# Optimization experiments

Hardware: AMD Instinct MI355X
Metric: run time of the kernel (lower is better)

Reference implementation:

```python
import jax, jax.numpy as jnp
import numpy as np

# Hardcoded capability requirements per task (3 capabilities x 13 tasks), as in the source.
CAP_MATRIX = 0.01 * np.array([
    [0.0, 33.0, 50.0, 43.0, 56.0, 67.0, 62.0, 47.0, 50.0, 51.0, 64.0, 64.0, 68.0],
    [0.0, 33.0, 49.0, 39.0, 58.0, 67.0, 60.0, 54.0, 52.0, 52.0, 67.0, 69.0, 71.0],
    [0.0, 33.0, 42.0, 39.0, 44.0, 52.0, 49.0, 42.0, 45.0, 46.0, 52.0, 53.0, 56.0],
], dtype=np.float32)  # [3, 13]

T_TASKS = 64      # tasks per observation sequence
B_SEQS = 262144   # number of observation sequences
N_TASK_IDS = 13
CAP_DIM = 3


def setup_inputs() -> dict:
    key = jax.random.key(0)
    k1, k2, k3, k4, k5 = jax.random.split(key, 5)
    # Performance encoding must avoid the invalid (1,1) combo:
    # state 0 -> (0,0) no info; state 1 -> (0,1) success; state 2 -> (1,0) failure.
    state = jax.random.randint(k1, (T_TASKS, B_SEQS), 0, 3)
    inptasksperf = jnp.stack(
        [(state == 2).astype(jnp.int32), (state == 1).astype(jnp.int32)], axis=-1
    )  # [T, B, 2]
    tasksobsids = jax.random.randint(k2, (T_TASKS, B_SEQS, 1), 0, N_TASK_IDS).astype(jnp.int32)
    taskspredids = jax.random.randint(k3, (B_SEQS, 1), 0, N_TASK_IDS).astype(jnp.int32)
    inptasksobs = jnp.zeros((T_TASKS, B_SEQS, 1), jnp.float32)  # only shapes are used
    betas = 20.0 * jax.random.uniform(k4, (CAP_DIM,), jnp.float32)
    zetas = jax.random.uniform(k5, (CAP_DIM,), jnp.float32)
    return {
        "inptasksobs": inptasksobs,
        "inptasksperf": inptasksperf,
        "tasksobsids": tasksobsids,
        "taskspredids": taskspredids,
        "num_obs_tasks": T_TASKS,
        "betas": betas,
        "zetas": zetas,
    }


def reference(inptasksobs, inptasksperf, tasksobsids, taskspredids, num_obs_tasks, betas, zetas):
    cap_table = jnp.asarray(CAP_MATRIX.T)                # [13, 3] per-task capability rows
    obs_cap = cap_table[tasksobsids[..., 0]]             # [T, B, 3]
    p0 = inptasksperf[..., 0] != 0                       # [T, B]
    p1 = inptasksperf[..., 1] != 0
    success = jnp.logical_and(~p0, p1)                   # (0,1) -> success
    failure = jnp.logical_and(p0, ~p1)                   # (1,0) -> failure; (0,0) -> skip

    def step(cap, x):
        oc, s, f = x                                     # oc [B,3], s/f [B]
        cap = jnp.where(s[:, None], jnp.maximum(cap, oc), cap)
        cap = jnp.where(f[:, None], jnp.minimum(cap, oc), cap)
        return cap, None

    cap0 = jnp.zeros((obs_cap.shape[1], CAP_DIM), jnp.float32)
    cap, _ = jax.lax.scan(step, cap0, (obs_cap, success, failure))  # [B, 3]

    req = cap_table[taskspredids[:, 0]]                  # [B, 3]
    p = betas * (req - cap)                              # [B, 3]
    trust = jnp.prod((1.0 + jnp.exp(p)) ** (-zetas), axis=-1, keepdims=True)  # [B, 1]
    return trust
```

## Files before the change

### kernel.cpp

```cpp
#include <hip/hip_runtime.h>

#define T_TASKS 64
#define B_SEQS 262144
#define BLOCK 256
#define CHUNKS 4
#define TPC 16
#define PAIRS 64

#define POS_BIG  3.402823466e+38f
#define NEG_BIG -3.402823466e+38f

typedef int v4i __attribute__((ext_vector_type(4)));
typedef int v2i __attribute__((ext_vector_type(2)));

__constant__ float c_capT[13][4] = {
    {0.00f, 0.00f, 0.00f, 0.f}, {0.33f, 0.33f, 0.33f, 0.f},
    {0.50f, 0.49f, 0.42f, 0.f}, {0.43f, 0.39f, 0.39f, 0.f},
    {0.56f, 0.58f, 0.44f, 0.f}, {0.67f, 0.67f, 0.52f, 0.f},
    {0.62f, 0.60f, 0.49f, 0.f}, {0.47f, 0.54f, 0.42f, 0.f},
    {0.50f, 0.52f, 0.45f, 0.f}, {0.51f, 0.52f, 0.46f, 0.f},
    {0.64f, 0.67f, 0.52f, 0.f}, {0.64f, 0.69f, 0.53f, 0.f},
    {0.68f, 0.71f, 0.56f, 0.f},
};

#define STEP(l, h, A, B)                          \
    l = __builtin_amdgcn_fmed3f(l, A, B);         \
    h = __builtin_amdgcn_fmed3f(h, A, B);

#define GLOAD4(dst, ptr) \
    asm volatile("global_load_dwordx4 %0, %1, off" : "=v"(dst) : "v"(ptr))
#define GLOAD2(dst, ptr) \
    asm volatile("global_load_dwordx2 %0, %1, off" : "=v"(dst) : "v"(ptr))
#define WAITC(N)                                                  \
    asm volatile("s_waitcnt vmcnt(" #N ")" ::: "memory");         \
    __builtin_amdgcn_sched_barrier(0);

__global__ __launch_bounds__(BLOCK, 4) void trust_kernel(
    const v4i* __restrict__ perf2,
    const v2i* __restrict__ obs2,
    const int* __restrict__ predids,
    const float* __restrict__ betas,
    const float* __restrict__ zetas,
    float* __restrict__ out)
{
    __shared__ float4 s_cap[13];
    __shared__ float  s_lh[CHUNKS][2 * PAIRS][7];

    if (threadIdx.x < 13)
        s_cap[threadIdx.x] = *(const float4*)&c_capT[threadIdx.x][0];
    __syncthreads();

    const int tid = threadIdx.x;
    const int wv  = tid >> 6;
    const int ln  = tid & 63;
    const size_t RS = B_SEQS / 2;
    const size_t pairBase = (size_t)blockIdx.x * PAIRS;

    const v4i* ap = perf2 + (size_t)(wv * TPC) * RS + pairBase + ln;
    const v2i* bp = obs2  + (size_t)(wv * TPC) * RS + pairBase + ln;

    v4i pfs0, pfs1, pfs2, pfs3;
    v2i ids0, ids1, ids2, ids3;

#define ISSUE(S)                                   \
    GLOAD4(pfs##S, ap);  ap += RS;                 \
    GLOAD2(ids##S, bp);  bp += RS;

    float la0=NEG_BIG, la1=NEG_BIG, la2=NEG_BIG;
    float ha0=POS_BIG, ha1=POS_BIG, ha2=POS_BIG;
    float lb0=NEG_BIG, lb1=NEG_BIG, lb2=NEG_BIG;
    float hb0=POS_BIG, hb1=POS_BIG, hb2=POS_BIG;

#define CONSUME(pf, idv)                                                     \
    {                                                                        \
        const float4 oa = s_cap[(idv).x];                                    \
        const float4 ob = s_cap[(idv).y];                                    \
        const bool sa = ((pf).x == 0) && ((pf).y != 0);                      \
        const bool fa = ((pf).x != 0) && ((pf).y == 0);                      \
        const bool sb = ((pf).z == 0) && ((pf).w != 0);                      \
        const bool fb = ((pf).z != 0) && ((pf).w == 0);                      \
        const float Aa0 = sa ? oa.x : NEG_BIG, Ba0 = fa ? oa.x : POS_BIG;    \
        const float Aa1 = sa ? oa.y : NEG_BIG, Ba1 = fa ? oa.y : POS_BIG;    \
        const float Aa2 = sa ? oa.z : NEG_BIG, Ba2 = fa ? oa.z : POS_BIG;    \
        const float Ab0 = sb ? ob.x : NEG_BIG, Bb0 = fb ? ob.x : POS_BIG;    \
        const float Ab1 = sb ? ob.y : NEG_BIG, Bb1 = fb ? ob.y : POS_BIG;    \
        const float Ab2 = sb ? ob.z : NEG_BIG, Bb2 = fb ? ob.z : POS_BIG;    \
        STEP(la0, ha0, Aa0, Ba0)                                             \
        STEP(la1, ha1, Aa1, Ba1)                                             \
        STEP(la2, ha2, Aa2, Ba2)                                             \
        STEP(lb0, hb0, Ab0, Bb0)                                             \
        STEP(lb1, hb1, Ab1, Bb1)                                             \
        STEP(lb2, hb2, Ab2, Bb2)                                             \
    }

    ISSUE(0) ISSUE(1) ISSUE(2) ISSUE(3)
    WAITC(6) CONSUME(pfs0, ids0) ISSUE(0)
    WAITC(6) CONSUME(pfs1, ids1) ISSUE(1)
    WAITC(6) CONSUME(pfs2, ids2) ISSUE(2)
    WAITC(6) CONSUME(pfs3, ids3) ISSUE(3)
    WAITC(6) CONSUME(pfs0, ids0) ISSUE(0)
    WAITC(6) CONSUME(pfs1, ids1) ISSUE(1)
    WAITC(6) CONSUME(pfs2, ids2) ISSUE(2)
    WAITC(6) CONSUME(pfs3, ids3) ISSUE(3)
    WAITC(6) CONSUME(pfs0, ids0) ISSUE(0)
    WAITC(6) CONSUME(pfs1, ids1) ISSUE(1)
    WAITC(6) CONSUME(pfs2, ids2) ISSUE(2)
    WAITC(6) CONSUME(pfs3, ids3) ISSUE(3)
    WAITC(6) CONSUME(pfs0, ids0)
    WAITC(4) CONSUME(pfs1, ids1)
    WAITC(2) CONSUME(pfs2, ids2)
    WAITC(0) CONSUME(pfs3, ids3)
#undef CONSUME
#undef ISSUE

    float* da = &s_lh[wv][2 * ln][0];
    da[0]=la0; da[1]=la1; da[2]=la2; da[3]=ha0; da[4]=ha1; da[5]=ha2;
    float* db = &s_lh[wv][2 * ln + 1][0];
    db[0]=lb0; db[1]=lb1; db[2]=lb2; db[3]=hb0; db[4]=hb1; db[5]=hb2;
    __syncthreads();

    if (tid < 2 * PAIRS) {
        float x0 = 0.0f, x1 = 0.0f, x2 = 0.0f;
        #pragma unroll
        for (int cc = 0; cc < CHUNKS; ++cc) {
            const float* q = &s_lh[cc][tid][0];
            x0 = fminf(fmaxf(x0, q[0]), q[3]);
            x1 = fminf(fmaxf(x1, q[1]), q[4]);
            x2 = fminf(fmaxf(x2, q[2]), q[5]);
        }
        const size_t seq = (size_t)blockIdx.x * (2 * PAIRS) + tid;
        const int pid = predids[seq];
        const float4 r = s_cap[pid];

        const float q0 = betas[0] * (r.x - x0);
        const float q1 = betas[1] * (r.y - x1);
        const float q2 = betas[2] * (r.z - x2);

        const float t0 = powf(1.0f + expf(q0), -zetas[0]);
        const float t1 = powf(1.0f + expf(q1), -zetas[1]);
        const float t2 = powf(1.0f + expf(q2), -zetas[2]);

        out[seq] = t0 * t1 * t2;
    }
}

extern "C" void kernel_launch(void* const* d_in, const int* in_sizes, int n_in,
                              void* d_out, int out_size, void* d_ws, size_t ws_size,
                              hipStream_t stream) {
    const v4i*   perf2   = (const v4i*)d_in[1];
    const v2i*   obs2    = (const v2i*)d_in[2];
    const int*   predids = (const int*)d_in[3];
    const float* betas   = (const float*)d_in[5];
    const float* zetas   = (const float*)d_in[6];
    float* out = (float*)d_out;

    const int blocks = B_SEQS / (2 * PAIRS);
    trust_kernel<<<blocks, BLOCK, 0, stream>>>(perf2, obs2, predids, betas, zetas, out);
}
```

Baseline: 267.5 us.

## Process two pair-columns per thread to double work per block and halve grid

Doubles PAIRS so each thread handles two adjacent 64-pair column groups, issuing two loads per slot and keeping four sets of min/max accumulators, with pipeline depth reduced from four slots to two. The final reduction now uses all 256 threads instead of half. This aims to raise memory-level parallelism per wave and reduce block count and idle threads in the epilogue, at the cost of more registers and shared memory per block (occupancy risk at launch bounds 4).

```diff
diff --git a/kernel.cpp b/kernel.cpp
--- a/kernel.cpp
+++ b/kernel.cpp
@@ -5,7 +5,7 @@
 #define BLOCK 256
 #define CHUNKS 4
 #define TPC 16
-#define PAIRS 64
+#define PAIRS 128
 
 #define POS_BIG  3.402823466e+38f
 #define NEG_BIG -3.402823466e+38f
@@ -56,70 +56,86 @@
     const size_t RS = B_SEQS / 2;
     const size_t pairBase = (size_t)blockIdx.x * PAIRS;
 
-    const v4i* ap = perf2 + (size_t)(wv * TPC) * RS + pairBase + ln;
-    const v2i* bp = obs2  + (size_t)(wv * TPC) * RS + pairBase + ln;
+    const v4i* ap0 = perf2 + (size_t)(wv * TPC) * RS + pairBase + ln;
+    const v4i* ap1 = ap0 + 64;
+    const v2i* bp0 = obs2  + (size_t)(wv * TPC) * RS + pairBase + ln;
+    const v2i* bp1 = bp0 + 64;
 
-    v4i pfs0, pfs1, pfs2, pfs3;
-    v2i ids0, ids1, ids2, ids3;
+    v4i pfA0, pfB0, pfA1, pfB1;
+    v2i idA0, idB0, idA1, idB1;
 
-#define ISSUE(S)                                   \
-    GLOAD4(pfs##S, ap);  ap += RS;                 \
-    GLOAD2(ids##S, bp);  bp += RS;
+#define ISSUE(S)                                        \
+    GLOAD4(pfA##S, ap0);  GLOAD4(pfB##S, ap1);          \
+    ap0 += RS;  ap1 += RS;                              \
+    GLOAD2(idA##S, bp0);  GLOAD2(idB##S, bp1);          \
+    bp0 += RS;  bp1 += RS;
 
-    float la0=NEG_BIG, la1=NEG_BIG, la2=NEG_BIG;
-    float ha0=POS_BIG, ha1=POS_BIG, ha2=POS_BIG;
-    float lb0=NEG_BIG, lb1=NEG_BIG, lb2=NEG_BIG;
-    float hb0=POS_BIG, hb1=POS_BIG, hb2=POS_BIG;
+    float la0=NEG_BIG, la1=NEG_BIG, la2=NEG_BIG, ha0=POS_BIG, ha1=POS_BIG, ha2=POS_BIG;
+    float lb0=NEG_BIG, lb1=NEG_BIG, lb2=NEG_BIG, hb0=POS_BIG, hb1=POS_BIG, hb2=POS_BIG;
+    float lc0=NEG_BIG, lc1=NEG_BIG, lc2=NEG_BIG, hc0=POS_BIG, hc1=POS_BIG, hc2=POS_BIG;
+    float ld0=NEG_BIG, ld1=NEG_BIG, ld2=NEG_BIG, hd0=POS_BIG, hd1=POS_BIG, hd2=POS_BIG;
 
-#define CONSUME(pf, idv)                                                     \
+#define CONSUME12(pf, idv, l0,l1,l2,h0,h1,h2, m0,m1,m2,g0,g1,g2)             \
     {                                                                        \
         const float4 oa = s_cap[(idv).x];                                    \
         const float4 ob = s_cap[(idv).y];                                    \
-        const bool sa = ((pf).x == 0) && ((pf).y != 0);                      \
-        const bool fa = ((pf).x != 0) && ((pf).y == 0);                      \
-        const bool sb = ((pf).z == 0) && ((pf).w != 0);                      \
-        const bool fb = ((pf).z != 0) && ((pf).w == 0);                      \
-        const float Aa0 = sa ? oa.x : NEG_BIG, Ba0 = fa ? oa.x : POS_BIG;    \
-        const float Aa1 = sa ? oa.y : NEG_BIG, Ba1 = fa ? oa.y : POS_BIG;    \
-        const float Aa2 = sa ? oa.z : NEG_BIG, Ba2 = fa ? oa.z : POS_BIG;    \
-        const float Ab0 = sb ? ob.x : NEG_BIG, Bb0 = fb ? ob.x : POS_BIG;    \
-        const float Ab1 = sb ? ob.y : NEG_BIG, Bb1 = fb ? ob.y : POS_BIG;    \
-        const float Ab2 = sb ? ob.z : NEG_BIG, Bb2 = fb ? ob.z : POS_BIG;    \
-        STEP(la0, ha0, Aa0, Ba0)                                             \
-        STEP(la1, ha1, Aa1, Ba1)                                             \
-        STEP(la2, ha2, Aa2, Ba2)                                             \
-        STEP(lb0, hb0, Ab0, Bb0)                                             \
-        STEP(lb1, hb1, Ab1, Bb1)                                             \
-        STEP(lb2, hb2, Ab2, Bb2)                                             \
+        const bool sx = ((pf).x == 0) && ((pf).y != 0);                      \
+        const bool fx = ((pf).x != 0) && ((pf).y == 0);                      \
+        const bool sy = ((pf).z == 0) && ((pf).w != 0);                      \
+        const bool fy = ((pf).z != 0) && ((pf).w == 0);                      \
+        const float Ax0 = sx ? oa.x : NEG_BIG, Bx0 = fx ? oa.x : POS_BIG;    \
+        const float Ax1 = sx ? oa.y : NEG_BIG, Bx1 = fx ? oa.y : POS_BIG;    \
+        const float Ax2 = sx ? oa.z : NEG_BIG, Bx2 = fx ? oa.z : POS_BIG;    \
+        const float Ay0 = sy ? ob.x : NEG_BIG, By0 = fy ? ob.x : POS_BIG;    \
+        const float Ay1 = sy ? ob.y : NEG_BIG, By1 = fy ? ob.y : POS_BIG;    \
+        const float Ay2 = sy ? ob.z : NEG_BIG, By2 = fy ? ob.z : POS_BIG;    \
+        STEP(l0, h0, Ax0, Bx0)                                               \
+        STEP(l1, h1, Ax1, Bx1)                                               \
+        STEP(l2, h2, Ax2, Bx2)                                               \
+        STEP(m0, g0, Ay0, By0)                                               \
+        STEP(m1, g1, Ay1, By1)                                               \
+        STEP(m2, g2, Ay2, By2)                                               \
     }
 
-    ISSUE(0) ISSUE(1) ISSUE(2) ISSUE(3)
-    WAITC(6) CONSUME(pfs0, ids0) ISSUE(0)
-    WAITC(6) CONSUME(pfs1, ids1) ISSUE(1)
-    WAITC(6) CONSUME(pfs2, ids2) ISSUE(2)
-    WAITC(6) CONSUME(pfs3, ids3) ISSUE(3)
-    WAITC(6) CONSUME(pfs0, ids0) ISSUE(0)
-    WAITC(6) CONSUME(pfs1, ids1) ISSUE(1)
-    WAITC(6) CONSUME(pfs2, ids2) ISSUE(2)
-    WAITC(6) CONSUME(pfs3, ids3) ISSUE(3)
-    WAITC(6) CONSUME(pfs0, ids0) ISSUE(0)
-    WAITC(6) CONSUME(pfs1, ids1) ISSUE(1)
-    WAITC(6) CONSUME(pfs2, ids2) ISSUE(2)
-    WAITC(6) CONSUME(pfs3, ids3) ISSUE(3)
-    WAITC(6) CONSUME(pfs0, ids0)
-    WAITC(4) CONSUME(pfs1, ids1)
-    WAITC(2) CONSUME(pfs2, ids2)
-    WAITC(0) CONSUME(pfs3, ids3)
-#undef CONSUME
+#define CONSUME_SLOT(S)                                                          \
+    CONSUME12(pfA##S, idA##S, la0,la1,la2,ha0,ha1,ha2, lb0,lb1,lb2,hb0,hb1,hb2)  \
+    CONSUME12(pfB##S, idB##S, lc0,lc1,lc2,hc0,hc1,hc2, ld0,ld1,ld2,hd0,hd1,hd2)
+
+    ISSUE(0) ISSUE(1)
+    WAITC(4) CONSUME_SLOT(0) ISSUE(0)
+    WAITC(4) CONSUME_SLOT(1) ISSUE(1)
+    WAITC(4) CONSUME_SLOT(0) ISSUE(0)
+    WAITC(4) CONSUME_SLOT(1) ISSUE(1)
+    WAITC(4) CONSUME_SLOT(0) ISSUE(0)
+    WAITC(4) CONSUME_SLOT(1) ISSUE(1)
+    WAITC(4) CONSUME_SLOT(0) ISSUE(0)
+    WAITC(4) CONSUME_SLOT(1) ISSUE(1)
+    WAITC(4) CONSUME_SLOT(0) ISSUE(0)
+    WAITC(4) CONSUME_SLOT(1) ISSUE(1)
+    WAITC(4) CONSUME_SLOT(0) ISSUE(0)
+    WAITC(4) CONSUME_SLOT(1) ISSUE(1)
+    WAITC(4) CONSUME_SLOT(0) ISSUE(0)
+    WAITC(4) CONSUME_SLOT(1) ISSUE(1)
+    WAITC(4) CONSUME_SLOT(0)
+    WAITC(0) CONSUME_SLOT(1)
+#undef CONSUME_SLOT
+#undef CONSUME12
 #undef ISSUE
 
-    float* da = &s_lh[wv][2 * ln][0];
-    da[0]=la0; da[1]=la1; da[2]=la2; da[3]=ha0; da[4]=ha1; da[5]=ha2;
-    float* db = &s_lh[wv][2 * ln + 1][0];
-    db[0]=lb0; db[1]=lb1; db[2]=lb2; db[3]=hb0; db[4]=hb1; db[5]=hb2;
+    {
+        float* p;
+        p = &s_lh[wv][2 * ln][0];
+        p[0]=la0; p[1]=la1; p[2]=la2; p[3]=ha0; p[4]=ha1; p[5]=ha2;
+        p = &s_lh[wv][2 * ln + 1][0];
+        p[0]=lb0; p[1]=lb1; p[2]=lb2; p[3]=hb0; p[4]=hb1; p[5]=hb2;
+        p = &s_lh[wv][128 + 2 * ln][0];
+        p[0]=lc0; p[1]=lc1; p[2]=lc2; p[3]=hc0; p[4]=hc1; p[5]=hc2;
+        p = &s_lh[wv][129 + 2 * ln][0];
+        p[0]=ld0; p[1]=ld1; p[2]=ld2; p[3]=hd0; p[4]=hd1; p[5]=hd2;
+    }
     __syncthreads();
 
-    if (tid < 2 * PAIRS) {
+    {
         float x0 = 0.0f, x1 = 0.0f, x2 = 0.0f;
         #pragma unroll
         for (int cc = 0; cc < CHUNKS; ++cc) {
```

New measurement: 271.2 us. No clear change (+1.4%).
